# Kernel tuning notes

Measured on AMD Instinct MI355X. Metric: run time of the kernel, lower is better.

## Reference

```python
import jax, jax.numpy as jnp
import numpy as np

B, S, D, H, F = 2, 1024, 768, 12, 6
DH = D // H  # 64


def setup_inputs() -> dict:
    key = jax.random.key(0)
    ks = jax.random.split(key, 10)
    s = 0.02
    return {
        "x": jax.random.normal(ks[0], (B, S, D), jnp.float32),
        "W_kv": jax.random.normal(ks[1], (D, 2 * D), jnp.float32) * s,
        "b_kv": jnp.zeros((2 * D,), jnp.float32),
        "W_q": jax.random.normal(ks[2], (F, D, D), jnp.float32) * s,
        "b_q": jnp.zeros((F, D), jnp.float32),
        "W_m1": jax.random.normal(ks[3], (F * D, 2 * D), jnp.float32) * s,
        "b_m1": jnp.zeros((2 * D,), jnp.float32),
        "W_m2": jax.random.normal(ks[4], (2 * D, F * D), jnp.float32) * s,
        "b_m2": jnp.zeros((F * D,), jnp.float32),
        "cross_scale": jnp.asarray(0.1, jnp.float32),
        "W_g1": jax.random.normal(ks[5], (D, F * D // 4), jnp.float32) * s,
        "b_g1": jnp.zeros((F * D // 4,), jnp.float32),
        "W_g2": jax.random.normal(ks[6], (F * D // 4, F), jnp.float32) * s,
        "b_g2": jnp.zeros((F,), jnp.float32),
        "W_out": jax.random.normal(ks[7], (D, D), jnp.float32) * s,
        "b_out": jnp.zeros((D,), jnp.float32),
        "ln_g": jnp.ones((D,), jnp.float32),
        "ln_b": jnp.zeros((D,), jnp.float32),
    }


def reference(x, W_kv, b_kv, W_q, b_q, W_m1, b_m1, W_m2, b_m2, cross_scale,
              W_g1, b_g1, W_g2, b_g2, W_out, b_out, ln_g, ln_b):
    b, s, d = x.shape
    # shared K/V projection (single GEMM)
    kv = x @ W_kv + b_kv
    k, v = jnp.split(kv, 2, axis=-1)
    k = k.reshape(b, s, H, DH).transpose(0, 2, 1, 3)  # [B,H,S,DH]
    v = v.reshape(b, s, H, DH).transpose(0, 2, 1, 3)
    # all 6 frame queries in one batched GEMM
    q = jnp.einsum('bsd,fde->bfse', x, W_q) + b_q[None, :, None, :]
    q = q.reshape(b, F, s, H, DH).transpose(0, 1, 3, 2, 4)  # [B,F,H,S,DH]
    # per-frame attention sharing K/V (grouped-query style)
    attn = jnp.einsum('bfhsd,bhtd->bfhst', q, k) / jnp.sqrt(jnp.float32(DH))
    attn = jax.nn.softmax(attn, axis=-1)
    out = jnp.einsum('bfhst,bhtd->bfhsd', attn, v)  # [B,F,H,S,DH]
    # concat frames along last dim, frame-major (matches torch.cat order)
    stacked = out.transpose(0, 3, 1, 2, 4).reshape(b, s, F * d)
    # cross-frame MLP mixing (exact GELU as in torch default)
    h1 = jax.nn.gelu(stacked @ W_m1 + b_m1, approximate=False)
    mixed = stacked + cross_scale * (h1 @ W_m2 + b_m2)
    # frame gating
    g1 = jax.nn.gelu(x @ W_g1 + b_g1, approximate=False)
    gates = jax.nn.softmax(g1 @ W_g2 + b_g2, axis=-1)  # [B,S,F]
    combined = jnp.einsum('bsfd,bsf->bsd', mixed.reshape(b, s, F, d), gates)
    combined = combined @ W_out + b_out
    y = x + combined
    mu = jnp.mean(y, axis=-1, keepdims=True)
    var = jnp.var(y, axis=-1, keepdims=True)
    return (y - mu) / jnp.sqrt(var + 1e-5) * ln_g + ln_b
```

## Files before the change

kernel.cpp:

```cpp
#include <hip/hip_runtime.h>
#include <hip/hip_bf16.h>

#define B_ 2
#define S_ 1024
#define D_ 768
#define H_ 12
#define F_ 6
#define DH_ 64
#define BS_ (B_*S_)
#define D2_ (2*D_)
#define FD_ (F_*D_)
#define FD4_ (FD_/4)

typedef __attribute__((ext_vector_type(8))) short bf16x8;
typedef __attribute__((ext_vector_type(4))) short bf16x4;
typedef __attribute__((ext_vector_type(4))) float f32x4;

__device__ __forceinline__ float gelu_exact(float x) {
    return 0.5f * x * (1.0f + erff(x * 0.70710678118654752f));
}

__device__ __forceinline__ short f2bf(float f) {
    union { float f; unsigned u; } v; v.f = f;
    unsigned r = v.u + 0x7fff + ((v.u >> 16) & 1);
    return (short)(r >> 16);
}
__device__ __forceinline__ short f2bf_t(float f) {
    return (short)(__float_as_uint(f) >> 16);
}
__device__ __forceinline__ float bf2f(short b) {
    union { unsigned u; float f; } v;
    v.u = ((unsigned)(unsigned short)b) << 16;
    return v.f;
}
__device__ __forceinline__ float fast_exp2(float x) {
#if __has_builtin(__builtin_amdgcn_exp2f)
    return __builtin_amdgcn_exp2f(x);
#else
    float r; asm("v_exp_f32 %0, %1" : "=v"(r) : "v"(x)); return r;
#endif
}


#define GEMM_STAGE_A16(av)                                                    \
    {                                                                         \
        _Pragma("unroll")                                                     \
        for (int c = 0; c < 4; c++) {                                         \
            const int kc = (akb >> 3) + c;                                    \
            *(bf16x8*)&As[((amt*8 + kc)*16 + ((ar15 ^ kc ^ amt) & 15))*8] = (av)[c]; \
        }                                                                     \
    }

#define GEMM_STAGE_B16(bv)                                                    \
    {                                                                         \
        _Pragma("unroll")                                                     \
        for (int j = 0; j < 4; j++) {                                         \
            const int n  = bn0 + j;                                           \
            const int nt = n >> 4;                                            \
            bf16x8 s;                                                         \
            _Pragma("unroll")                                                 \
            for (int r = 0; r < 8; r++) s[r] = (bv)[r][j];                    \
            *(bf16x8*)&Bs[((nt*8 + bkg)*16 + (((n & 15) ^ bkg ^ nt) & 15))*8] = s; \
        }                                                                     \
    }

#define GEMM_LOAD_A16(av, kb)                                                 \
    {                                                                         \
        _Pragma("unroll")                                                     \
        for (int c = 0; c < 4; c++)                                           \
            (av)[c] = *(const bf16x8*)(Ap + (kb) + c*8);                      \
    }

#define GEMM_LOAD_B16(bv, kb, strideN)                                        \
    {                                                                         \
        _Pragma("unroll")                                                     \
        for (int r = 0; r < 8; r++)                                           \
            *(bf16x4*)&(bv)[r][0] = *(const bf16x4*)(Wp + (long)((kb) + r) * (strideN)); \
    }

#define GEMM_COMPUTE()                                                        \
    {                                                                         \
        _Pragma("unroll")                                                     \
        for (int ks = 0; ks < 2; ks++) {                                      \
            const int kc = ks*4 + quad;                                       \
            bf16x8 af[4], bf[4];                                              \
            _Pragma("unroll")                                                 \
            for (int mt = 0; mt < 4; mt++) {                                  \
                const int MT = wr*4 + mt;                                     \
                af[mt] = *(const bf16x8*)&As[((MT*8 + kc)*16 + ((l15 ^ kc ^ MT) & 15))*8]; \
            }                                                                 \
            _Pragma("unroll")                                                 \
            for (int nt = 0; nt < 4; nt++) {                                  \
                const int NT = wc*4 + nt;                                     \
                bf[nt] = *(const bf16x8*)&Bs[((NT*8 + kc)*16 + ((l15 ^ kc ^ NT) & 15))*8]; \
            }                                                                 \
            _Pragma("unroll")                                                 \
            for (int mt = 0; mt < 4; mt++)                                    \
                _Pragma("unroll")                                             \
                for (int nt = 0; nt < 4; nt++)                                \
                    acc[mt][nt] = __builtin_amdgcn_mfma_f32_16x16x32_bf16(    \
                        af[mt], bf[nt], acc[mt][nt], 0, 0, 0);                \
        }                                                                     \
    }

#define GEMM_COMMON_IDS()                                                     \
    const int tid  = threadIdx.x;                                             \
    const int wave = tid >> 6;                                                \
    const int lane = tid & 63;                                                \
    const int l15  = lane & 15;                                               \
    const int quad = lane >> 4;                                               \
    const int wr   = wave >> 1;                                               \
    const int wc   = wave & 1;                                                \
    const int ar   = tid >> 1;                                                \
    const int akb  = (tid & 1) * 32;                                          \
    const int amt  = ar >> 4;                                                 \
    const int ar15 = ar & 15;                                                 \
    const int bn0  = (tid & 31) * 4;                                          \
    const int bkg  = tid >> 5;

template<int B16>
__device__ __forceinline__ void gemm_load_b(
    const void* __restrict__ Wv, long rowOff, int N, int kb,
    float bf[8][4], short bh[8][4])
{
    if constexpr (B16) {
        const short* Wp = (const short*)Wv + rowOff;
        #pragma unroll
        for (int r = 0; r < 8; r++)
            *(bf16x4*)&bh[r][0] = *(const bf16x4*)(Wp + (long)(kb + r) * N);
    } else {
        const float* Wp = (const float*)Wv + rowOff;
        #pragma unroll
        for (int r = 0; r < 8; r++)
            *(float4*)&bf[r][0] = *(const float4*)(Wp + (long)(kb + r) * N);
    }
}

template<int B16>
__device__ __forceinline__ void gemm_stage_b(
    short* Bs, int bn0, int bkg, const float bf[8][4], const short bh[8][4])
{
    #pragma unroll
    for (int j = 0; j < 4; j++) {
        const int n  = bn0 + j;
        const int nt = n >> 4;
        bf16x8 s;
        #pragma unroll
        for (int r = 0; r < 8; r++) s[r] = B16 ? bh[r][j] : f2bf_t(bf[r][j]);
        *(bf16x8*)&Bs[((nt*8 + bkg)*16 + (((n & 15) ^ bkg ^ nt) & 15))*8] = s;
    }
}

#define PPK_N0 393216
#define PPK_N1 294912
#define PPK_N2 884736
#define PPK_N3 221184
#define PPK_N4 1769472
__global__ __launch_bounds__(256) void prepack(
    const float* __restrict__ x, const float* __restrict__ Wkv,
    const float* __restrict__ Wq, const float* __restrict__ Wg1,
    const float* __restrict__ Wm1,
    short* __restrict__ xb, short* __restrict__ wkvb,
    short* __restrict__ wqb, short* __restrict__ wg1b,
    short* __restrict__ wmb)
{
    long idx = (long)blockIdx.x * 256 + threadIdx.x;
    const float* src; short* dst;
    if (idx < PPK_N0) { src = x; dst = xb; }
    else if ((idx -= PPK_N0) < PPK_N1) { src = Wkv; dst = wkvb; }
    else if ((idx -= PPK_N1) < PPK_N2) { src = Wq;  dst = wqb; }
    else if ((idx -= PPK_N2) < PPK_N3) { src = Wg1; dst = wg1b; }
    else { idx -= PPK_N3; src = Wm1; dst = wmb; }
    float4 v = ((const float4*)src)[idx];
    bf16x4 o;
    o[0] = f2bf(v.x); o[1] = f2bf(v.y); o[2] = f2bf(v.z); o[3] = f2bf(v.w);
    ((bf16x4*)dst)[idx] = o;
}

__global__ __launch_bounds__(256) void prepack_w2(
    const float* __restrict__ Wm2, short* __restrict__ wmb)
{
    long idx = (long)blockIdx.x * 256 + threadIdx.x;
    float4 v = ((const float4*)Wm2)[idx];
    bf16x4 o;
    o[0] = f2bf(v.x); o[1] = f2bf(v.y); o[2] = f2bf(v.z); o[3] = f2bf(v.w);
    ((bf16x4*)wmb)[idx] = o;
}

template<int MODE, int B16, int OUT16>
__global__ __launch_bounds__(256, 2) void mfma_gemm(
    const short* __restrict__ A, const void* __restrict__ Wv,
    const float* __restrict__ bias, void* __restrict__ Cv,
    int M, int N, int K, int kLen,
    long cStrideZ, long kStrideZ,
    const short* __restrict__ addend, const float* __restrict__ scale_ptr)
{
    short* C16 = (short*)Cv;
    float* C32 = (float*)Cv;
    if (blockIdx.z) { C16 += blockIdx.z * cStrideZ; C32 += blockIdx.z * cStrideZ; }
    const int kBeg = (int)(blockIdx.z * kStrideZ);
    const int kEnd = kBeg + kLen;

    __shared__ __align__(16) short As[8192];
    __shared__ __align__(16) short Bs[8192];

    GEMM_COMMON_IDS();

    const int m0 = blockIdx.y * 128;
    const int n0 = blockIdx.x * 128;

    const short* Ap = A + (long)(m0 + ar) * K + akb;
    const long wRowOff = (long)(bkg * 8) * N + n0 + bn0;

    f32x4 acc[4][4];
    #pragma unroll
    for (int i = 0; i < 4; i++)
        #pragma unroll
        for (int j = 0; j < 4; j++)
            acc[i][j] = (f32x4){0.f, 0.f, 0.f, 0.f};

    bf16x8 a0[4], a1[4];
    float bf0[8][4], bf1[8][4];
    short bh0[8][4], bh1[8][4];
    GEMM_LOAD_A16(a0, kBeg);
    gemm_load_b<B16>(Wv, wRowOff, N, kBeg, bf0, bh0);

    for (int kb = kBeg; kb < kEnd; kb += 128) {
        GEMM_STAGE_A16(a0);
        gemm_stage_b<B16>(Bs, bn0, bkg, bf0, bh0);
        __syncthreads();
        GEMM_LOAD_A16(a1, kb + 64);
        gemm_load_b<B16>(Wv, wRowOff, N, kb + 64, bf1, bh1);
        GEMM_COMPUTE();
        __syncthreads();
        GEMM_STAGE_A16(a1);
        gemm_stage_b<B16>(Bs, bn0, bkg, bf1, bh1);
        __syncthreads();
        if (kb + 128 < kEnd) {
            GEMM_LOAD_A16(a0, kb + 128);
            gemm_load_b<B16>(Wv, wRowOff, N, kb + 128, bf0, bh0);
        }
        GEMM_COMPUTE();
        __syncthreads();
    }

    float scale = 0.0f;
    if (MODE == 2) scale = *scale_ptr;
    #pragma unroll
    for (int nt = 0; nt < 4; nt++) {
        const int col = n0 + wc*64 + nt*16 + l15;
        const float bcol = (MODE == 4) ? 0.0f : bias[col];
        #pragma unroll
        for (int mt = 0; mt < 4; mt++) {
            #pragma unroll
            for (int r = 0; r < 4; r++) {
                const long row = m0 + wr*64 + mt*16 + quad*4 + r;
                float v = acc[mt][nt][r] + bcol;
                if (MODE == 2) v = bf2f(addend[row*N + col]) + scale * v;
                if (OUT16) C16[row*N + col] = f2bf(v);
                else       C32[row*N + col] = v;
            }
        }
    }
}

#define QSCALE 0.18033688011112042f
__global__ __launch_bounds__(256, 2) void xproj_gemm(
    const short* __restrict__ xb,
    const short* __restrict__ W_kv, const float* __restrict__ b_kv, float* __restrict__ bufKV,
    const short* __restrict__ W_q,  const float* __restrict__ b_q,  short* __restrict__ qb,
    const short* __restrict__ W_g1, const float* __restrict__ b_g1, float* __restrict__ bufG1)
{
    __shared__ __align__(16) short As[8192];
    __shared__ __align__(16) short Bs[8192];

    GEMM_COMMON_IDS();

    const int ntile = blockIdx.x;
    const int m0 = blockIdx.y * 128;

    const short* Wseg; const float* bseg; float* Cseg = nullptr;
    int Nw, ncol, fidx = 0, mode;
    if (ntile < 12) {
        Wseg = W_kv; bseg = b_kv; Cseg = bufKV; Nw = 1536; ncol = ntile * 128; mode = 0;
    } else if (ntile < 48) {
        const int t = ntile - 12; fidx = t / 6;
        ncol = (t % 6) * 128;
        Wseg = W_q + (long)fidx * D_ * D_; bseg = b_q + fidx * D_;
        Nw = 768; mode = 1;
    } else {
        const int t = ntile - 48;
        Wseg = W_g1; bseg = b_g1; Cseg = bufG1; Nw = 1152; ncol = t * 128; mode = 2;
    }

    const short* Ap = xb + (long)(m0 + ar) * D_ + akb;
    const short* Wp = Wseg + (long)(bkg * 8) * Nw + ncol + bn0;

    f32x4 acc[4][4];
    #pragma unroll
    for (int i = 0; i < 4; i++)
        #pragma unroll
        for (int j = 0; j < 4; j++)
            acc[i][j] = (f32x4){0.f, 0.f, 0.f, 0.f};

    bf16x8 a0[4], a1[4];
    short b0[8][4], b1[8][4];
    GEMM_LOAD_A16(a0, 0);
    GEMM_LOAD_B16(b0, 0, Nw);

    for (int kb = 0; kb < D_; kb += 128) {
        GEMM_STAGE_A16(a0); GEMM_STAGE_B16(b0);
        __syncthreads();
        GEMM_LOAD_A16(a1, kb + 64);
        GEMM_LOAD_B16(b1, kb + 64, Nw);
        GEMM_COMPUTE();
        __syncthreads();
        GEMM_STAGE_A16(a1); GEMM_STAGE_B16(b1);
        __syncthreads();
        if (kb + 128 < D_) {
            GEMM_LOAD_A16(a0, kb + 128);
            GEMM_LOAD_B16(b0, kb + 128, Nw);
        }
        GEMM_COMPUTE();
        __syncthreads();
    }

    if (mode == 1) {
        const int bb = m0 >> 10;
        const int sBase = (m0 & 1023) + wr*64;
        #pragma unroll
        for (int nt = 0; nt < 4; nt++) {
            const int col = ncol + wc*64 + nt*16 + l15;
            const int hh = col >> 6, dd = col & 63;
            const float bcol = bseg[col];
            short* qBase = qb + ((((long)fidx*B_ + bb)*H_ + hh)*S_)*64 + dd;
            #pragma unroll
            for (int mt = 0; mt < 4; mt++) {
                #pragma unroll
                for (int r = 0; r < 4; r++) {
                    const int s = sBase + mt*16 + quad*4 + r;
                    qBase[(long)s*64] = f2bf((acc[mt][nt][r] + bcol) * QSCALE);
                }
            }
        }
    } else {
        #pragma unroll
        for (int nt = 0; nt < 4; nt++) {
            const int col = ncol + wc*64 + nt*16 + l15;
            const float bcol = bseg[col];
            #pragma unroll
            for (int mt = 0; mt < 4; mt++) {
                #pragma unroll
                for (int r = 0; r < 4; r++) {
                    const long row = m0 + wr*64 + mt*16 + quad*4 + r;
                    float v = acc[mt][nt][r] + bcol;
                    if (mode == 2) v = gelu_exact(v);
                    Cseg[row*Nw + col] = v;
                }
            }
        }
    }
}

__global__ __launch_bounds__(256) void repack_kv(
    const float* __restrict__ kvf, short* __restrict__ Kb, short* __restrict__ Vtb)
{
    __shared__ __align__(16) short T[64*64];
    const int bx = blockIdx.x;
    const int st = bx & 15;
    const int h  = (bx >> 4) % 12;
    const int b  = bx / 192;
    const int tid = threadIdx.x;
    const int s_loc = tid & 63;
    const int dch  = (tid >> 6) * 16;
    const int s0 = st * 64;

    const float* kr = kvf + (long)(b*S_ + s0 + s_loc) * D2_ + h*64 + dch;
    float v[16];

    #pragma unroll
    for (int i = 0; i < 4; i++) *(float4*)&v[i*4] = *(const float4*)(kr + i*4);
    {
        short* kw = Kb + ((long)(b*H_ + h)*S_ + s0 + s_loc)*64 + dch;
        bf16x8 p0, p1;
        #pragma unroll
        for (int i = 0; i < 8; i++) { p0[i] = f2bf(v[i]); p1[i] = f2bf(v[8+i]); }
        *(bf16x8*)&kw[0] = p0;
        *(bf16x8*)&kw[8] = p1;
    }

    #pragma unroll
    for (int i = 0; i < 4; i++) *(float4*)&v[i*4] = *(const float4*)(kr + D_ + i*4);
    #pragma unroll
    for (int i = 0; i < 16; i++) {
        const int d = dch + i;
        T[d*64 + ((((s_loc >> 3) ^ d) & 7) << 3) + (s_loc & 7)] = f2bf(v[i]);
    }
    __syncthreads();
    const int d_loc = tid >> 2;
    const int sc = (tid & 3) * 16;
    const int c0 = sc >> 3;
    bf16x8 o0 = *(const bf16x8*)&T[d_loc*64 + (((c0 ^ d_loc) & 7) << 3)];
    bf16x8 o1 = *(const bf16x8*)&T[d_loc*64 + ((((c0+1) ^ d_loc) & 7) << 3)];
    short* vw = Vtb + ((long)(b*H_ + h)*64 + d_loc)*S_ + s0 + sc;
    *(bf16x8*)&vw[0] = o0;
    *(bf16x8*)&vw[8] = o1;
}

__global__ __launch_bounds__(256, 4) void attn_mfma8(
    const short* __restrict__ qb,
    const short* __restrict__ Kb,
    const short* __restrict__ Vt,
    short* __restrict__ stackedb)
{
    __shared__ __align__(16) short Ks[64*64];
    __shared__ __align__(16) short Vs[64*64];
    __shared__ __align__(16) short Ps[4][16*64];

    const int bx = blockIdx.x;
    const int qt = bx & 15;
    const int rest = bx >> 4;
    const int h = rest % 12;
    const int r2 = rest / 12;
    const int f = r2 % 6;
    const int b = r2 / 6;

    const int tid  = threadIdx.x;
    const int wave = tid >> 6;
    const int lane = tid & 63;
    const int l15  = lane & 15;
    const int quad = lane >> 4;

    const short* Kg = Kb + (long)(b*H_ + h) * S_ * 64;
    const short* Vg = Vt + (long)(b*H_ + h) * 64 * S_;

    bf16x8 aq[2];
    {
        const short* qp = qb + ((((long)f*B_ + b)*H_ + h)*S_ + qt*64 + wave*16)*64;
        #pragma unroll
        for (int ks = 0; ks < 2; ks++)
            aq[ks] = *(const bf16x8*)&qp[l15*64 + ks*32 + quad*8];
    }

    bf16x8 onesf;
    {
        const short ONE = (short)0x3F80;
        #pragma unroll
        for (int j = 0; j < 8; j++) onesf[j] = (l15 == 0) ? ONE : (short)0;
    }

    const int skey = tid >> 2;
    const int sch  = (tid & 3) * 2;

    short* Psw = Ps[wave];

    f32x4 st[4], o[4], lo;
    lo = (f32x4){0.f,0.f,0.f,0.f};
    #pragma unroll
    for (int nt = 0; nt < 4; nt++) o[nt] = (f32x4){0.f,0.f,0.f,0.f};

    bf16x8 kc[2], vc[2], kn[2], vn[2];
    #pragma unroll
    for (int j = 0; j < 2; j++) {
        const int ch = sch + j;
        kc[j] = *(const bf16x8*)&Kg[(long)skey*64 + ch*8];
        vc[j] = *(const bf16x8*)&Vg[(long)skey*S_ + ch*8];
    }

    for (int kt = 0; kt < 16; kt++) {
        #pragma unroll
        for (int j = 0; j < 2; j++) {
            const int ch = sch + j;
            const int slot = ((ch ^ skey) & 7) << 3;
            *(bf16x8*)&Ks[skey*64 + slot] = kc[j];
            *(bf16x8*)&Vs[skey*64 + slot] = vc[j];
        }
        __syncthreads();

        if (kt + 1 < 16) {
            #pragma unroll
            for (int j = 0; j < 2; j++) {
                const int ch = sch + j;
                kn[j] = *(const bf16x8*)&Kg[(long)((kt+1)*64 + skey)*64 + ch*8];
                vn[j] = *(const bf16x8*)&Vg[(long)skey*S_ + (kt+1)*64 + ch*8];
            }
        }

        #pragma unroll
        for (int nt = 0; nt < 4; nt++) st[nt] = (f32x4){0.f,0.f,0.f,0.f};
        #pragma unroll
        for (int nt = 0; nt < 4; nt++) {
            const int key = nt*16 + l15;
            #pragma unroll
            for (int ks = 0; ks < 2; ks++) {
                const bf16x8 kf = *(const bf16x8*)
                    &Ks[key*64 + ((((ks*4 + quad) ^ key) & 7) << 3)];
                st[nt] = __builtin_amdgcn_mfma_f32_16x16x32_bf16(aq[ks], kf, st[nt], 0, 0, 0);
            }
        }

        #pragma unroll
        for (int r = 0; r < 4; r++) {
            const int row = quad*4 + r;
            #pragma unroll
            for (int nt = 0; nt < 4; nt++) {
                const float p = fast_exp2(st[nt][r]);
                const int col = nt*16 + l15;
                Psw[row*64 + ((((col >> 3) ^ row) & 7) << 3) + (col & 7)] = f2bf_t(p);
            }
        }

        bf16x8 pa[2];
        #pragma unroll
        for (int ks = 0; ks < 2; ks++)
            pa[ks] = *(const bf16x8*)
                &Psw[l15*64 + ((((ks*4 + quad) ^ l15) & 7) << 3)];

        #pragma unroll
        for (int nt = 0; nt < 4; nt++) {
            const int dim = nt*16 + l15;
            #pragma unroll
            for (int ks = 0; ks < 2; ks++) {
                const bf16x8 vf = *(const bf16x8*)
                    &Vs[dim*64 + ((((ks*4 + quad) ^ dim) & 7) << 3)];
                o[nt] = __builtin_amdgcn_mfma_f32_16x16x32_bf16(pa[ks], vf, o[nt], 0, 0, 0);
            }
        }
        #pragma unroll
        for (int ks = 0; ks < 2; ks++)
            lo = __builtin_amdgcn_mfma_f32_16x16x32_bf16(pa[ks], onesf, lo, 0, 0, 0);

        __syncthreads();
        #pragma unroll
        for (int j = 0; j < 2; j++) { kc[j] = kn[j]; vc[j] = vn[j]; }
    }

    float inv[4];
    #pragma unroll
    for (int r = 0; r < 4; r++)
        inv[r] = 1.0f / __shfl(lo[r], quad << 4);
    const long rowBase = (long)(b*S_ + qt*64 + wave*16 + quad*4);
    #pragma unroll
    for (int nt = 0; nt < 4; nt++) {
        #pragma unroll
        for (int r = 0; r < 4; r++) {
            stackedb[(rowBase + r)*FD_ + f*D_ + h*64 + nt*16 + l15] =
                f2bf(o[nt][r] * inv[r]);
        }
    }
}

__global__ __launch_bounds__(64) void gates_kernel(
    const float* __restrict__ g1, const float* __restrict__ W_g2,
    const float* __restrict__ b_g2, float* __restrict__ gates)
{
    const int m = blockIdx.x;
    const int lane = threadIdx.x;
    float p[6] = {0.f,0.f,0.f,0.f,0.f,0.f};
    for (int k = lane; k < FD4_; k += 64) {
        float g = g1[(long)m*FD4_ + k];
        #pragma unroll
        for (int f = 0; f < 6; f++) p[f] += g * W_g2[k*6 + f];
    }
    #pragma unroll
    for (int f = 0; f < 6; f++) {
        float v = p[f];
        #pragma unroll
        for (int off = 1; off < 64; off <<= 1) v += __shfl_xor(v, off);
        p[f] = v + b_g2[f];
    }
    float mx = p[0];
    #pragma unroll
    for (int f = 1; f < 6; f++) mx = fmaxf(mx, p[f]);
    float se = 0.f;
    #pragma unroll
    for (int f = 0; f < 6; f++) { p[f] = expf(p[f] - mx); se += p[f]; }
    const float inv = 1.0f / se;
    if (lane < 6) gates[m*6 + lane] = p[lane] * inv;
}

__global__ __launch_bounds__(256) void reduce_m1(
    const short* __restrict__ p, const float* __restrict__ bias,
    short* __restrict__ out)
{
    const int idx = blockIdx.x * 256 + threadIdx.x;
    const int col4 = idx % (D2_/4);
    const long MN4 = (long)BS_ * D2_ / 4;
    bf16x4 a = ((const bf16x4*)p)[idx];
    bf16x4 b = ((const bf16x4*)p)[idx + MN4];
    bf16x4 c = ((const bf16x4*)p)[idx + 2*MN4];
    float4 bb = ((const float4*)bias)[col4];
    bf16x4 o;
    o[0] = f2bf(gelu_exact(bf2f(a[0]) + bf2f(b[0]) + bf2f(c[0]) + bb.x));
    o[1] = f2bf(gelu_exact(bf2f(a[1]) + bf2f(b[1]) + bf2f(c[1]) + bb.y));
    o[2] = f2bf(gelu_exact(bf2f(a[2]) + bf2f(b[2]) + bf2f(c[2]) + bb.z));
    o[3] = f2bf(gelu_exact(bf2f(a[3]) + bf2f(b[3]) + bf2f(c[3]) + bb.w));
    ((bf16x4*)out)[idx] = o;
}

__global__ __launch_bounds__(256) void combine_kernel(
    const short* __restrict__ mixedb, const float* __restrict__ gates,
    short* __restrict__ comb)
{
    const int idx = blockIdx.x * 256 + threadIdx.x;
    const int m = idx / 192;
    const int d4 = idx - m*192;
    const bf16x4* mrow = (const bf16x4*)(mixedb + (long)m * FD_);
    float4 a = {0.f,0.f,0.f,0.f};
    #pragma unroll
    for (int f = 0; f < 6; f++) {
        float g = gates[m*6 + f];
        bf16x4 v = mrow[f*192 + d4];
        a.x += g*bf2f(v[0]); a.y += g*bf2f(v[1]);
        a.z += g*bf2f(v[2]); a.w += g*bf2f(v[3]);
    }
    bf16x4 o;
    o[0] = f2bf(a.x); o[1] = f2bf(a.y); o[2] = f2bf(a.z); o[3] = f2bf(a.w);
    ((bf16x4*)comb)[idx] = o;
}

__global__ __launch_bounds__(256) void reduce_ln(
    const float* __restrict__ p, const float* __restrict__ bias,
    const float* __restrict__ x,
    const float* __restrict__ ln_g, const float* __restrict__ ln_b,
    float* __restrict__ out)
{
    __shared__ float red[8];
    const int m = blockIdx.x;
    const int tid = threadIdx.x;
    const long MN = (long)BS_ * D_;
    float vals[3];
    float s = 0.f, s2 = 0.f;
    #pragma unroll
    for (int i = 0; i < 3; i++) {
        const int d = tid + 256*i;
        const long o = (long)m*D_ + d;
        float v = x[o] + p[o] + p[MN + o] + bias[d];
        vals[i] = v;
        s += v; s2 += v*v;
    }
    #pragma unroll
    for (int off = 32; off >= 1; off >>= 1) {
        s  += __shfl_xor(s, off);
        s2 += __shfl_xor(s2, off);
    }
    const int wave = tid >> 6;
    if ((tid & 63) == 0) { red[wave*2] = s; red[wave*2+1] = s2; }
    __syncthreads();
    s  = red[0]+red[2]+red[4]+red[6];
    s2 = red[1]+red[3]+red[5]+red[7];
    const float mu  = s * (1.0f/D_);
    const float var = s2 * (1.0f/D_) - mu*mu;
    const float inv = rsqrtf(var + 1e-5f);
    #pragma unroll
    for (int i = 0; i < 3; i++) {
        const int d = tid + 256*i;
        out[(long)m*D_ + d] = (vals[i] - mu) * inv * ln_g[d] + ln_b[d];
    }
}

extern "C" void kernel_launch(void* const* d_in, const int* in_sizes, int n_in,
                              void* d_out, int out_size, void* d_ws, size_t ws_size,
                              hipStream_t stream)
{
    const float* x     = (const float*)d_in[0];
    const float* W_kv  = (const float*)d_in[1];
    const float* b_kv  = (const float*)d_in[2];
    const float* W_q   = (const float*)d_in[3];
    const float* b_q   = (const float*)d_in[4];
    const float* W_m1  = (const float*)d_in[5];
    const float* b_m1  = (const float*)d_in[6];
    const float* W_m2  = (const float*)d_in[7];
    const float* b_m2  = (const float*)d_in[8];
    const float* cross = (const float*)d_in[9];
    const float* W_g1  = (const float*)d_in[10];
    const float* b_g1  = (const float*)d_in[11];
    const float* W_g2  = (const float*)d_in[12];
    const float* b_g2  = (const float*)d_in[13];
    const float* W_out = (const float*)d_in[14];
    const float* b_out = (const float*)d_in[15];
    const float* ln_g  = (const float*)d_in[16];
    const float* ln_b  = (const float*)d_in[17];
    float* out = (float*)d_out;

    float* ws       = (float*)d_ws;
    float* bufA     = ws;
    float* bufB     = bufA + (size_t)4718592;
    short* stackedS = (short*)(bufB + (size_t)3145728);
    float* bufC     = (float*)(stackedS + (size_t)BS_*FD_);
    float* gates    = bufC + (size_t)BS_*FD4_;

    short* wpack = (short*)(gates + 12288);
    short* xb    = wpack;
    short* wkvb  = xb + (size_t)BS_*D_;
    short* wqb   = wkvb + (size_t)D_*D2_;
    short* wg1b  = wqb + (size_t)F_*D_*D_;
    short* wmb   = wg1b + (size_t)D_*FD4_;

    short* qb      = (short*)bufA;
    short* m1part  = (short*)bufA;
    short* mixedb  = (short*)bufA;
    short* Kb      = (short*)bufC;
    short* Vt      = Kb + (size_t)B_*H_*S_*DH_;
    short* h1b     = (short*)bufB;
    short* combb   = (short*)bufC;
    float* outPart = (float*)stackedS;

    dim3 blk(256);

    prepack<<<dim3((PPK_N0+PPK_N1+PPK_N2+PPK_N3+PPK_N4)/256), blk, 0, stream>>>(
        x, W_kv, W_q, W_g1, W_m1, xb, wkvb, wqb, wg1b, wmb);
    xproj_gemm<<<dim3(57, 16, 1), blk, 0, stream>>>(
        xb, wkvb, b_kv, bufB, wqb, b_q, qb, wg1b, b_g1, bufC);
    gates_kernel<<<dim3(BS_), dim3(64), 0, stream>>>(bufC, W_g2, b_g2, gates);
    repack_kv<<<dim3(B_*H_*16), blk, 0, stream>>>(bufB, Kb, Vt);
    attn_mfma8<<<dim3(16 * 144), blk, 0, stream>>>(qb, Kb, Vt, stackedS);
    mfma_gemm<4,1,1><<<dim3(D2_/128, BS_/128, 3), blk, 0, stream>>>(
        stackedS, wmb, b_m1, m1part, BS_, D2_, FD_, FD_/3,
        (long)BS_*D2_, FD_/3, nullptr, nullptr);
    prepack_w2<<<dim3(1769472/256), blk, 0, stream>>>(W_m2, wmb);
    reduce_m1<<<dim3(BS_*D2_/4/256), blk, 0, stream>>>(m1part, b_m1, h1b);
    mfma_gemm<2,1,1><<<dim3(FD_/128, BS_/128, 1), blk, 0, stream>>>(
        h1b, wmb, b_m2, mixedb, BS_, FD_, D2_, D2_,
        0, 0, stackedS, cross);
    combine_kernel<<<dim3(BS_*(D_/4)/256), blk, 0, stream>>>(mixedb, gates, combb);
    mfma_gemm<4,0,0><<<dim3(D_/128, BS_/128, 2), blk, 0, stream>>>(
        combb, W_out, b_out, outPart, BS_, D_, D_, D_/2,
        (long)BS_*D_, D_/2, nullptr, nullptr);
    reduce_ln<<<dim3(BS_), blk, 0, stream>>>(outPart, b_out, x, ln_g, ln_b, out);
}
```

Baseline: 436.9 us.

## Double query rows per attention block to reuse K/V tiles across two row tiles

Each attention wave now processes two 16-row query tiles (128 query rows per block) instead of one, so every K/V tile staged in shared memory feeds twice as many MFMAs and the V fragments are reused across both row tiles. The grid is halved, which cuts global K/V traffic and per-tile barrier overhead. In exchange, register pressure rises (doubled accumulators and Q fragments) and fewer blocks give less parallelism to fill the GPU.

```diff
diff --git a/kernel.cpp b/kernel.cpp
--- a/kernel.cpp
+++ b/kernel.cpp
@@ -407,7 +407,7 @@
     *(bf16x8*)&vw[8] = o1;
 }
 
-__global__ __launch_bounds__(256, 4) void attn_mfma8(
+__global__ __launch_bounds__(256, 4) void attn_mfma9(
     const short* __restrict__ qb,
     const short* __restrict__ Kb,
     const short* __restrict__ Vt,
@@ -418,8 +418,8 @@
     __shared__ __align__(16) short Ps[4][16*64];
 
     const int bx = blockIdx.x;
-    const int qt = bx & 15;
-    const int rest = bx >> 4;
+    const int qt = bx & 7;
+    const int rest = bx >> 3;
     const int h = rest % 12;
     const int r2 = rest / 12;
     const int f = r2 % 6;
@@ -434,12 +434,14 @@
     const short* Kg = Kb + (long)(b*H_ + h) * S_ * 64;
     const short* Vg = Vt + (long)(b*H_ + h) * 64 * S_;
 
-    bf16x8 aq[2];
+    bf16x8 aq[2][2];
     {
-        const short* qp = qb + ((((long)f*B_ + b)*H_ + h)*S_ + qt*64 + wave*16)*64;
-        #pragma unroll
-        for (int ks = 0; ks < 2; ks++)
-            aq[ks] = *(const bf16x8*)&qp[l15*64 + ks*32 + quad*8];
+        const short* qp = qb + ((((long)f*B_ + b)*H_ + h)*S_ + qt*128 + wave*32)*64;
+        #pragma unroll
+        for (int rt = 0; rt < 2; rt++)
+            #pragma unroll
+            for (int ks = 0; ks < 2; ks++)
+                aq[rt][ks] = *(const bf16x8*)&qp[(rt*16 + l15)*64 + ks*32 + quad*8];
     }
 
     bf16x8 onesf;
@@ -454,10 +456,13 @@
 
     short* Psw = Ps[wave];
 
-    f32x4 st[4], o[4], lo;
-    lo = (f32x4){0.f,0.f,0.f,0.f};
-    #pragma unroll
-    for (int nt = 0; nt < 4; nt++) o[nt] = (f32x4){0.f,0.f,0.f,0.f};
+    f32x4 o[2][4], lo[2];
+    #pragma unroll
+    for (int rt = 0; rt < 2; rt++) {
+        lo[rt] = (f32x4){0.f,0.f,0.f,0.f};
+        #pragma unroll
+        for (int nt = 0; nt < 4; nt++) o[rt][nt] = (f32x4){0.f,0.f,0.f,0.f};
+    }
 
     bf16x8 kc[2], vc[2], kn[2], vn[2];
     #pragma unroll
@@ -486,35 +491,38 @@
             }
         }
 
-        #pragma unroll
-        for (int nt = 0; nt < 4; nt++) st[nt] = (f32x4){0.f,0.f,0.f,0.f};
-        #pragma unroll
-        for (int nt = 0; nt < 4; nt++) {
-            const int key = nt*16 + l15;
-            #pragma unroll
-            for (int ks = 0; ks < 2; ks++) {
-                const bf16x8 kf = *(const bf16x8*)
-                    &Ks[key*64 + ((((ks*4 + quad) ^ key) & 7) << 3)];
-                st[nt] = __builtin_amdgcn_mfma_f32_16x16x32_bf16(aq[ks], kf, st[nt], 0, 0, 0);
+        bf16x8 pa[2][2];
+        #pragma unroll
+        for (int rt = 0; rt < 2; rt++) {
+            f32x4 st[4];
+            #pragma unroll
+            for (int nt = 0; nt < 4; nt++) st[nt] = (f32x4){0.f,0.f,0.f,0.f};
+            #pragma unroll
+            for (int nt = 0; nt < 4; nt++) {
+                const int key = nt*16 + l15;
+                #pragma unroll
+                for (int ks = 0; ks < 2; ks++) {
+                    const bf16x8 kf = *(const bf16x8*)
+                        &Ks[key*64 + ((((ks*4 + quad) ^ key) & 7) << 3)];
+                    st[nt] = __builtin_amdgcn_mfma_f32_16x16x32_bf16(
+                        aq[rt][ks], kf, st[nt], 0, 0, 0);
+                }
             }
-        }
-
-        #pragma unroll
-        for (int r = 0; r < 4; r++) {
-            const int row = quad*4 + r;
-            #pragma unroll
-            for (int nt = 0; nt < 4; nt++) {
-                const float p = fast_exp2(st[nt][r]);
-                const int col = nt*16 + l15;
-                Psw[row*64 + ((((col >> 3) ^ row) & 7) << 3) + (col & 7)] = f2bf_t(p);
+            #pragma unroll
+            for (int r = 0; r < 4; r++) {
+                const int row = quad*4 + r;
+                #pragma unroll
+                for (int nt = 0; nt < 4; nt++) {
+                    const float p = fast_exp2(st[nt][r]);
+                    const int col = nt*16 + l15;
+                    Psw[row*64 + ((((col >> 3) ^ row) & 7) << 3) + (col & 7)] = f2bf_t(p);
+                }
             }
-        }
-
-        bf16x8 pa[2];
-        #pragma unroll
-        for (int ks = 0; ks < 2; ks++)
-            pa[ks] = *(const bf16x8*)
-                &Psw[l15*64 + ((((ks*4 + quad) ^ l15) & 7) << 3)];
+            #pragma unroll
+            for (int ks = 0; ks < 2; ks++)
+                pa[rt][ks] = *(const bf16x8*)
+                    &Psw[l15*64 + ((((ks*4 + quad) ^ l15) & 7) << 3)];
+        }
 
         #pragma unroll
         for (int nt = 0; nt < 4; nt++) {
@@ -523,29 +531,35 @@
             for (int ks = 0; ks < 2; ks++) {
                 const bf16x8 vf = *(const bf16x8*)
                     &Vs[dim*64 + ((((ks*4 + quad) ^ dim) & 7) << 3)];
-                o[nt] = __builtin_amdgcn_mfma_f32_16x16x32_bf16(pa[ks], vf, o[nt], 0, 0, 0);
+                o[0][nt] = __builtin_amdgcn_mfma_f32_16x16x32_bf16(pa[0][ks], vf, o[0][nt], 0, 0, 0);
+                o[1][nt] = __builtin_amdgcn_mfma_f32_16x16x32_bf16(pa[1][ks], vf, o[1][nt], 0, 0, 0);
             }
         }
         #pragma unroll
-        for (int ks = 0; ks < 2; ks++)
-            lo = __builtin_amdgcn_mfma_f32_16x16x32_bf16(pa[ks], onesf, lo, 0, 0, 0);
+        for (int ks = 0; ks < 2; ks++) {
+            lo[0] = __builtin_amdgcn_mfma_f32_16x16x32_bf16(pa[0][ks], onesf, lo[0], 0, 0, 0);
+            lo[1] = __builtin_amdgcn_mfma_f32_16x16x32_bf16(pa[1][ks], onesf, lo[1], 0, 0, 0);
+        }
 
         __syncthreads();
         #pragma unroll
         for (int j = 0; j < 2; j++) { kc[j] = kn[j]; vc[j] = vn[j]; }
     }
 
-    float inv[4];
-    #pragma unroll
-    for (int r = 0; r < 4; r++)
-        inv[r] = 1.0f / __shfl(lo[r], quad << 4);
-    const long rowBase = (long)(b*S_ + qt*64 + wave*16 + quad*4);
-    #pragma unroll
-    for (int nt = 0; nt < 4; nt++) {
-        #pragma unroll
-        for (int r = 0; r < 4; r++) {
-            stackedb[(rowBase + r)*FD_ + f*D_ + h*64 + nt*16 + l15] =
-                f2bf(o[nt][r] * inv[r]);
+    #pragma unroll
+    for (int rt = 0; rt < 2; rt++) {
+        float inv[4];
+        #pragma unroll
+        for (int r = 0; r < 4; r++)
+            inv[r] = 1.0f / __shfl(lo[rt][r], quad << 4);
+        const long rowBase = (long)(b*S_ + qt*128 + wave*32 + rt*16 + quad*4);
+        #pragma unroll
+        for (int nt = 0; nt < 4; nt++) {
+            #pragma unroll
+            for (int r = 0; r < 4; r++) {
+                stackedb[(rowBase + r)*FD_ + f*D_ + h*64 + nt*16 + l15] =
+                    f2bf(o[rt][nt][r] * inv[r]);
+            }
         }
     }
 }
@@ -714,7 +728,7 @@
         xb, wkvb, b_kv, bufB, wqb, b_q, qb, wg1b, b_g1, bufC);
     gates_kernel<<<dim3(BS_), dim3(64), 0, stream>>>(bufC, W_g2, b_g2, gates);
     repack_kv<<<dim3(B_*H_*16), blk, 0, stream>>>(bufB, Kb, Vt);
-    attn_mfma8<<<dim3(16 * 144), blk, 0, stream>>>(qb, Kb, Vt, stackedS);
+    attn_mfma9<<<dim3(8 * 144), blk, 0, stream>>>(qb, Kb, Vt, stackedS);
     mfma_gemm<4,1,1><<<dim3(D2_/128, BS_/128, 3), blk, 0, stream>>>(
         stackedS, wmb, b_m1, m1part, BS_, D2_, FD_, FD_/3,
         (long)BS_*D2_, FD_/3, nullptr, nullptr);
```

Result: no change. 443.0 us (+1.4%).
